# Optimization experiments

Hardware: AMD Instinct MI355X
Metric: run time of the kernel (lower is better)

The kernel has to match this reference:

```python
import jax, jax.numpy as jnp
import numpy as np

DIM = 1024
HEADS = 32
HEAD_DIM = DIM // HEADS
SR_RATIO = 2
N_RATIO = SR_RATIO * SR_RATIO  # AvgPool1d kernel/stride
BN_EPS = 1e-6


def setup_inputs() -> dict:
    key = jax.random.key(0)
    ks = jax.random.split(key, 10)
    B, N, C = 4, 2048, DIM
    s = C ** -0.5
    return {
        "x": jax.random.normal(ks[0], (B, N, C), dtype=jnp.float32),
        # torch.nn.Linear weights, shape [out, in]; applied as x @ W.T
        "Wq": jax.random.normal(ks[1], (C, C), dtype=jnp.float32) * s,
        "Wk": jax.random.normal(ks[2], (C, C), dtype=jnp.float32) * s,
        "Wv": jax.random.normal(ks[3], (C, C), dtype=jnp.float32) * s,
        "Wp": jax.random.normal(ks[4], (C, C), dtype=jnp.float32) * s,
        "bp": jax.random.normal(ks[5], (C,), dtype=jnp.float32) * 0.01,
        # BatchNorm1d (eval mode) affine + running stats over channel dim C
        "bn_gamma": jnp.ones((C,), dtype=jnp.float32),
        "bn_beta": jnp.zeros((C,), dtype=jnp.float32),
        "bn_mean": jax.random.normal(ks[6], (C,), dtype=jnp.float32) * 0.01,
        "bn_var": jnp.ones((C,), dtype=jnp.float32) + jax.random.uniform(ks[7], (C,), dtype=jnp.float32) * 0.1,
    }


def reference(x, Wq, Wk, Wv, Wp, bp, bn_gamma, bn_beta, bn_mean, bn_var):
    B, N, C = x.shape
    scale = HEAD_DIM ** -0.5
    # Q from full-resolution tokens
    q = (x @ Wq.T).reshape(B, N, HEADS, HEAD_DIM).transpose(0, 2, 1, 3)  # [B,H,N,d]
    # spatial reduction: AvgPool1d(kernel=N_RATIO, stride=N_RATIO) over tokens
    xr = x.reshape(B, N // N_RATIO, N_RATIO, C).mean(axis=2)  # [B,M,C]
    # BatchNorm1d eval: normalize channel dim with running stats
    xr = (xr - bn_mean) * jax.lax.rsqrt(bn_var + BN_EPS) * bn_gamma + bn_beta
    M = xr.shape[1]
    k = (xr @ Wk.T).reshape(B, M, HEADS, HEAD_DIM).transpose(0, 2, 1, 3)  # [B,H,M,d]
    v = (xr @ Wv.T).reshape(B, M, HEADS, HEAD_DIM).transpose(0, 2, 1, 3)  # [B,H,M,d]
    # NOTE: no softmax in the original module — raw scaled scores feed the second matmul
    attn = jnp.einsum("bhnd,bhmd->bhnm", q, k) * scale  # [B,H,N,M]
    out = jnp.einsum("bhnm,bhmd->bhnd", attn, v)        # [B,H,N,d]
    out = out.transpose(0, 2, 1, 3).reshape(B, N, C)
    return out @ Wp.T + bp
```

## Files before the change

### kernel.cpp

```cpp
#include <hip/hip_runtime.h>
#include <stdint.h>

#define DEVFN __device__ __forceinline__

typedef __attribute__((ext_vector_type(8))) short s16x8;
typedef __attribute__((ext_vector_type(4))) float f32x4;

DEVFN float bf2f(uint16_t u) {
  union { uint32_t i; float f; } v; v.i = ((uint32_t)u) << 16; return v.f;
}
DEVFN uint16_t f2bf(float f) {
  union { float f; uint32_t i; } v; v.f = f;
  uint32_t u = v.i;
  return (uint16_t)((u + 0x7FFFu + ((u >> 16) & 1u)) >> 16);
}

DEVFN void gload_lds16(const void* g, void* l) {
  __builtin_amdgcn_global_load_lds(
      (const __attribute__((address_space(1))) uint32_t*)g,
      (__attribute__((address_space(3))) uint32_t*)l, 16, 0, 0);
}

__global__ __launch_bounds__(256)
void prep_kernel(const float* __restrict__ x,
                 const float* __restrict__ bn_g, const float* __restrict__ bn_b,
                 const float* __restrict__ bn_m, const float* __restrict__ bn_v,
                 const float* __restrict__ Wk, const float* __restrict__ Wv,
                 const float* __restrict__ Wp,
                 uint16_t* __restrict__ Xh,
                 uint16_t* __restrict__ XRh,
                 uint16_t* __restrict__ Wkvh,
                 uint16_t* __restrict__ Wph)
{
  const int t = threadIdx.x;
  const int bid = blockIdx.x;
  if (bid < 2048) {
    const int prow = bid;
    const int c0 = t * 4;
    const size_t xbase = (size_t)prow * 4096 + c0;
    float s[4] = {0.f, 0.f, 0.f, 0.f};
#pragma unroll
    for (int r = 0; r < 4; ++r) {
      const float4 w = *(const float4*)(x + xbase + (size_t)r * 1024);
      const float vv[4] = { w.x, w.y, w.z, w.w };
      uint64_t wh = 0;
#pragma unroll
      for (int j = 0; j < 4; ++j) {
        wh |= ((uint64_t)f2bf(vv[j])) << (16 * j);
        s[j] += vv[j];
      }
      *(uint64_t*)(Xh + xbase + (size_t)r * 1024) = wh;
    }
    uint64_t wh = 0;
#pragma unroll
    for (int j = 0; j < 4; ++j) {
      const int c = c0 + j;
      const float y = (s[j] * 0.25f - bn_m[c]) / sqrtf(bn_v[c] + 1e-6f) * bn_g[c] + bn_b[c];
      wh |= ((uint64_t)f2bf(y)) << (16 * j);
    }
    *(uint64_t*)(XRh + (size_t)prow * 1024 + c0) = wh;
  } else {
    const int wb = bid - 2048;
    const int which = wb >> 10;
    const int i = (wb & 1023) * 256 + t;
    const float* src = (which == 0) ? Wk : (which == 1) ? Wv : Wp;
    const float4 v = ((const float4*)src)[i];
    const float vv[4] = { v.x, v.y, v.z, v.w };
    uint64_t wh = 0;
#pragma unroll
    for (int j = 0; j < 4; ++j)
      wh |= ((uint64_t)f2bf(vv[j])) << (16 * j);
    if (which == 2) {
      ((uint64_t*)Wph)[i] = wh;
    } else {
      ((uint64_t*)Wkvh)[(size_t)which * (1024 * 1024 / 4) + i] = wh;
    }
  }
}

template<bool BATCHB, bool AMODA, int EPI, bool KSPLIT2>
__global__ __launch_bounds__(256, 3)
void gemm_nt(const uint16_t* __restrict__ A0,
             const uint16_t* __restrict__ B0,
             float* __restrict__ C32, uint16_t* __restrict__ Cb0,
             const float* __restrict__ bias,
             int M, int N, int K, int rows_per_batch)
{
  constexpr int BM = 64, BN = 128, BK = 128;
  constexpr int NREP = 2;
  constexpr int APASS = 4;
  constexpr int BPASS = 8;
  __shared__ uint16_t sA[BM * BK];
  __shared__ uint16_t sB[BN * BK];

  const int t = threadIdx.x;
  const int lane = t & 63;
  const int wc = t >> 6;
  const int fq = lane >> 4, fr = lane & 15;

  const int nwg = gridDim.x;
  const int cpx = nwg >> 3;
  const int orig = blockIdx.x;
  const int swz = (orig & 7) * cpx + (orig >> 3);
  const int nbx = N >> 7;
  const int bm = (swz / nbx) * BM;
  const int bn = (swz % nbx) * BN;

  const uint16_t* Ap = A0;
  const uint16_t* Bp = B0;
  if (BATCHB)
    Bp += (size_t)(bm / rows_per_batch) * (size_t)N * (size_t)K;
  if (KSPLIT2) {
    const size_t half = (size_t)blockIdx.y * M * N;
    if (EPI == 1) Cb0 += half; else C32 += half;
  }

  f32x4 acc[4][NREP];
#pragma unroll
  for (int m = 0; m < 4; ++m)
#pragma unroll
    for (int n = 0; n < NREP; ++n) acc[m][n] = (f32x4)0.0f;

  const int nkt = K >> (KSPLIT2 ? 8 : 7);
  const int kt0 = KSPLIT2 ? (blockIdx.y * nkt) : 0;
  for (int kt = kt0; kt < kt0 + nkt; ++kt) {
    __syncthreads();
#pragma unroll
    for (int i = 0; i < APASS; ++i) {
      const int X = t * 16 + i * 4096;
      const int r = X >> 8;
      const int g = ((X >> 4) & 15) ^ (r & 7);
      const int kcol = (kt << 7) + g * 8;
      const int arow = AMODA ? ((bm + r) & 1023) : (bm + r);
      gload_lds16(Ap + (size_t)arow * K + kcol, (char*)(&sA[0]) + X);
    }
#pragma unroll
    for (int i = 0; i < BPASS; ++i) {
      const int X = t * 16 + i * 4096;
      const int r = X >> 8;
      const int g = ((X >> 4) & 15) ^ (r & 7);
      const int kcol = (kt << 7) + g * 8;
      gload_lds16(Bp + (size_t)(bn + r) * K + kcol, (char*)(&sB[0]) + X);
    }
    __syncthreads();
#pragma unroll
    for (int ks = 0; ks < 4; ++ks) {
      s16x8 av[4], bv[NREP];
#pragma unroll
      for (int m = 0; m < 4; ++m) {
        const int ra = m * 16 + fr;
        const int offA = ra * 256 + ((((ks << 2) + fq) ^ (ra & 7)) << 4);
        av[m] = *(const s16x8*)((const char*)(&sA[0]) + offA);
      }
#pragma unroll
      for (int n = 0; n < NREP; ++n) {
        const int rb = wc * 32 + n * 16 + fr;
        const int offB = rb * 256 + ((((ks << 2) + fq) ^ (rb & 7)) << 4);
        bv[n] = *(const s16x8*)((const char*)(&sB[0]) + offB);
      }
#pragma unroll
      for (int m = 0; m < 4; ++m)
#pragma unroll
        for (int n = 0; n < NREP; ++n)
          acc[m][n] = __builtin_amdgcn_mfma_f32_16x16x32_bf16(
              av[m], bv[n], acc[m][n], 0, 0, 0);
    }
  }

#pragma unroll
  for (int m = 0; m < 4; ++m) {
#pragma unroll
    for (int n = 0; n < NREP; ++n) {
#pragma unroll
      for (int j = 0; j < 4; ++j) {
        const int row = bm + m * 16 + fq * 4 + j;
        const int col = bn + wc * 32 + n * 16 + fr;
        const size_t idx = (size_t)row * N + col;
        float v = acc[m][n][j];
        if constexpr (EPI == 0) {
          C32[idx] = v;
        } else if constexpr (EPI == 1) {
          Cb0[idx] = f2bf(v);
        } else {
          C32[idx] = v + bias[col];
        }
      }
    }
  }
}

__global__ __launch_bounds__(256)
void kv1_kernel(const uint16_t* __restrict__ KVcat, float* __restrict__ part)
{
  const int bid = blockIdx.x;
  const int bh = bid >> 3, ch = bid & 7;
  const int b = bh >> 5, h = bh & 31;
  const int t = threadIdx.x;
  __shared__ float sK[64][32];
  __shared__ float sV[64][32];
  const int f = t >> 3, e0 = (t & 7) * 4;
  const int lr = t >> 2, q = t & 3;
  const size_t rowb = (size_t)(b * 512 + ch * 64 + lr) * 2048 + h * 32 + q * 8;
  const size_t H = (size_t)2048 * 2048;
  const s16x8 k0 = *(const s16x8*)(KVcat + rowb);
  const s16x8 k1 = *(const s16x8*)(KVcat + H + rowb);
  const s16x8 v0 = *(const s16x8*)(KVcat + rowb + 1024);
  const s16x8 v1 = *(const s16x8*)(KVcat + H + rowb + 1024);
#pragma unroll
  for (int j = 0; j < 8; ++j) {
    sK[lr][q * 8 + j] = bf2f((uint16_t)k0[j]) + bf2f((uint16_t)k1[j]);
    sV[lr][q * 8 + j] = bf2f((uint16_t)v0[j]) + bf2f((uint16_t)v1[j]);
  }
  __syncthreads();
  float a0 = 0.f, a1 = 0.f, a2 = 0.f, a3 = 0.f;
#pragma unroll 16
  for (int mm = 0; mm < 64; ++mm) {
    const float kf = sK[mm][f];
    const float4 vv = *(const float4*)&sV[mm][e0];
    a0 += kf * vv.x; a1 += kf * vv.y; a2 += kf * vv.z; a3 += kf * vv.w;
  }
  float* o = part + ((size_t)bid * 32 + f) * 32 + e0;
  o[0] = a0; o[1] = a1; o[2] = a2; o[3] = a3;
}

__global__ __launch_bounds__(256)
void t_kernel(const float* __restrict__ part, const float* __restrict__ Wq,
              uint16_t* __restrict__ Tth)
{
  const int bid = blockIdx.x;
  const int b = bid >> 7, h = (bid >> 2) & 31, cc = bid & 3;
  const int bh = b * 32 + h;
  const int t = threadIdx.x;
  __shared__ float sKV[32][32];
  {
    const int f = t >> 3, e0 = (t & 7) * 4;
    f32x4 a = (f32x4)0.0f;
#pragma unroll
    for (int ch = 0; ch < 8; ++ch)
      a += *(const f32x4*)(part + ((size_t)(bh * 8 + ch) * 32 + f) * 32 + e0);
    a *= 0.17677669529663687f;
    *(f32x4*)&sKV[f][e0] = a;
  }
  __syncthreads();
  const int c = cc * 256 + t;
  f32x4 acc[8];
#pragma unroll
  for (int i = 0; i < 8; ++i) acc[i] = (f32x4)0.0f;
  const float* wqp = Wq + (size_t)(h * 32) * 1024 + c;
#pragma unroll 8
  for (int f = 0; f < 32; ++f) {
    const float wq = wqp[(size_t)f * 1024];
#pragma unroll
    for (int i = 0; i < 8; ++i) {
      const f32x4 kv = *(const f32x4*)&sKV[f][i * 4];
      acc[i] += kv * wq;
    }
  }
  const size_t o = (((size_t)b << 10) + c) * 1024 + h * 32;
#pragma unroll
  for (int i = 0; i < 8; ++i) {
    uint64_t wh = 0;
#pragma unroll
    for (int j = 0; j < 4; ++j)
      wh |= ((uint64_t)f2bf(acc[i][j])) << (16 * j);
    *(uint64_t*)(Tth + o + i * 4) = wh;
  }
}

extern "C" void kernel_launch(void* const* d_in, const int* in_sizes, int n_in,
                              void* d_out, int out_size, void* d_ws, size_t ws_size,
                              hipStream_t stream)
{
  const float* x   = (const float*)d_in[0];
  const float* Wq  = (const float*)d_in[1];
  const float* Wk  = (const float*)d_in[2];
  const float* Wv  = (const float*)d_in[3];
  const float* Wp  = (const float*)d_in[4];
  const float* bp  = (const float*)d_in[5];
  const float* bng = (const float*)d_in[6];
  const float* bnb = (const float*)d_in[7];
  const float* bnm = (const float*)d_in[8];
  const float* bnv = (const float*)d_in[9];
  float* out = (float*)d_out;

  char* ws = (char*)d_ws;
  size_t off = 0;
  auto alloc = [&](size_t bytes) {
    char* p = ws + off;
    off += (bytes + 255) & ~(size_t)255;
    return p;
  };
  uint16_t* Xh   = (uint16_t*)alloc((size_t)8192 * 1024 * 2);
  uint16_t* XRh  = (uint16_t*)alloc((size_t)2048 * 1024 * 2);
  uint16_t* Wkvh = (uint16_t*)alloc((size_t)2048 * 1024 * 2);
  uint16_t* Wph  = (uint16_t*)alloc((size_t)1024 * 1024 * 2);
  uint16_t* KVcat= (uint16_t*)alloc((size_t)2 * 2048 * 2048 * 2);
  uint16_t* Gh   = (uint16_t*)alloc((size_t)4096 * 1024 * 2);
  uint16_t* Tth = KVcat;
  float* KVpart = (float*)Gh;

  prep_kernel<<<5120, 256, 0, stream>>>(x, bng, bnb, bnm, bnv, Wk, Wv, Wp,
                                        Xh, XRh, Wkvh, Wph);
  gemm_nt<false, false, 1, true><<<dim3(512, 2), 256, 0, stream>>>(
      XRh, Wkvh, nullptr, KVcat, nullptr,
      2048, 2048, 1024, 1 << 30);
  kv1_kernel<<<1024, 256, 0, stream>>>(KVcat, KVpart);
  t_kernel<<<512, 256, 0, stream>>>(KVpart, Wq, Tth);
  gemm_nt<true, true, 1, false><<<512, 256, 0, stream>>>(
      Wph, Tth, nullptr, Gh, nullptr,
      4096, 1024, 1024, 1024);
  gemm_nt<true, false, 2, false><<<1024, 256, 0, stream>>>(
      Xh, Gh, out, nullptr, bp,
      8192, 1024, 1024, 2048);
}
```

Baseline: 94.26 us.

## Use 128-row GEMM tiles and overlap next-tile loads with MFMA compute

The GEMM kernel gains a SMALLM template option. The large GEMMs now use 128x128 tiles split across a 2x2 wave grid, while the small GEMM keeps 64-row tiles. The main loop now reads all fragments for a k-tile from LDS into registers, then issues the global-to-LDS loads for the next k-tile before running the MFMAs, so memory traffic overlaps with compute. The cost is more registers per thread (launch bounds lowered from 3 to 2 blocks per CU) and half as many workgroups on the 128-row launches.

```diff
diff --git a/kernel.cpp b/kernel.cpp
--- a/kernel.cpp
+++ b/kernel.cpp
@@ -78,24 +78,27 @@
   }
 }
 
-template<bool BATCHB, bool AMODA, int EPI, bool KSPLIT2>
-__global__ __launch_bounds__(256, 3)
+template<bool BATCHB, bool AMODA, int EPI, bool KSPLIT2, bool SMALLM>
+__global__ __launch_bounds__(256, 2)
 void gemm_nt(const uint16_t* __restrict__ A0,
              const uint16_t* __restrict__ B0,
              float* __restrict__ C32, uint16_t* __restrict__ Cb0,
              const float* __restrict__ bias,
              int M, int N, int K, int rows_per_batch)
 {
-  constexpr int BM = 64, BN = 128, BK = 128;
-  constexpr int NREP = 2;
-  constexpr int APASS = 4;
+  constexpr int BM = SMALLM ? 64 : 128, BN = 128, BK = 128;
+  constexpr int WCN = SMALLM ? 4 : 2;
+  constexpr int WNW = BN / WCN;
+  constexpr int NREP = WNW / 16;
+  constexpr int APASS = SMALLM ? 4 : 8;
   constexpr int BPASS = 8;
   __shared__ uint16_t sA[BM * BK];
   __shared__ uint16_t sB[BN * BK];
 
   const int t = threadIdx.x;
   const int lane = t & 63;
-  const int wc = t >> 6;
+  const int wave = t >> 6;
+  const int wr = wave / WCN, wc = wave % WCN;
   const int fq = lane >> 4, fr = lane & 15;
 
   const int nwg = gridDim.x;
@@ -121,10 +124,7 @@
 #pragma unroll
     for (int n = 0; n < NREP; ++n) acc[m][n] = (f32x4)0.0f;
 
-  const int nkt = K >> (KSPLIT2 ? 8 : 7);
-  const int kt0 = KSPLIT2 ? (blockIdx.y * nkt) : 0;
-  for (int kt = kt0; kt < kt0 + nkt; ++kt) {
-    __syncthreads();
+  auto STAGE = [&](int kt) {
 #pragma unroll
     for (int i = 0; i < APASS; ++i) {
       const int X = t * 16 + i * 4096;
@@ -142,29 +142,44 @@
       const int kcol = (kt << 7) + g * 8;
       gload_lds16(Bp + (size_t)(bn + r) * K + kcol, (char*)(&sB[0]) + X);
     }
+  };
+
+  const int nkt = K >> (KSPLIT2 ? 8 : 7);
+  const int kt0 = KSPLIT2 ? (blockIdx.y * nkt) : 0;
+  const int ktend = kt0 + nkt;
+
+  STAGE(kt0);
+  for (int kt = kt0; kt < ktend; ++kt) {
     __syncthreads();
+
+    s16x8 av[4][4], bv[4][NREP];
 #pragma unroll
     for (int ks = 0; ks < 4; ++ks) {
-      s16x8 av[4], bv[NREP];
 #pragma unroll
       for (int m = 0; m < 4; ++m) {
-        const int ra = m * 16 + fr;
+        const int ra = wr * 64 + m * 16 + fr;
         const int offA = ra * 256 + ((((ks << 2) + fq) ^ (ra & 7)) << 4);
-        av[m] = *(const s16x8*)((const char*)(&sA[0]) + offA);
+        av[ks][m] = *(const s16x8*)((const char*)(&sA[0]) + offA);
       }
 #pragma unroll
       for (int n = 0; n < NREP; ++n) {
-        const int rb = wc * 32 + n * 16 + fr;
+        const int rb = wc * WNW + n * 16 + fr;
         const int offB = rb * 256 + ((((ks << 2) + fq) ^ (rb & 7)) << 4);
-        bv[n] = *(const s16x8*)((const char*)(&sB[0]) + offB);
+        bv[ks][n] = *(const s16x8*)((const char*)(&sB[0]) + offB);
       }
+    }
+
+    __syncthreads();
+    if (kt + 1 < ktend) STAGE(kt + 1);
+
+#pragma unroll
+    for (int ks = 0; ks < 4; ++ks)
 #pragma unroll
       for (int m = 0; m < 4; ++m)
 #pragma unroll
         for (int n = 0; n < NREP; ++n)
           acc[m][n] = __builtin_amdgcn_mfma_f32_16x16x32_bf16(
-              av[m], bv[n], acc[m][n], 0, 0, 0);
-    }
+              av[ks][m], bv[ks][n], acc[m][n], 0, 0, 0);
   }
 
 #pragma unroll
@@ -173,8 +188,8 @@
     for (int n = 0; n < NREP; ++n) {
 #pragma unroll
       for (int j = 0; j < 4; ++j) {
-        const int row = bm + m * 16 + fq * 4 + j;
-        const int col = bn + wc * 32 + n * 16 + fr;
+        const int row = bm + wr * 64 + m * 16 + fq * 4 + j;
+        const int col = bn + wc * WNW + n * 16 + fr;
         const size_t idx = (size_t)row * N + col;
         float v = acc[m][n][j];
         if constexpr (EPI == 0) {
@@ -301,15 +316,15 @@
 
   prep_kernel<<<5120, 256, 0, stream>>>(x, bng, bnb, bnm, bnv, Wk, Wv, Wp,
                                         Xh, XRh, Wkvh, Wph);
-  gemm_nt<false, false, 1, true><<<dim3(512, 2), 256, 0, stream>>>(
+  gemm_nt<false, false, 1, true, false><<<dim3(256, 2), 256, 0, stream>>>(
       XRh, Wkvh, nullptr, KVcat, nullptr,
       2048, 2048, 1024, 1 << 30);
   kv1_kernel<<<1024, 256, 0, stream>>>(KVcat, KVpart);
   t_kernel<<<512, 256, 0, stream>>>(KVpart, Wq, Tth);
-  gemm_nt<true, true, 1, false><<<512, 256, 0, stream>>>(
+  gemm_nt<true, true, 1, false, true><<<512, 256, 0, stream>>>(
       Wph, Tth, nullptr, Gh, nullptr,
       4096, 1024, 1024, 1024);
-  gemm_nt<true, false, 2, false><<<1024, 256, 0, stream>>>(
+  gemm_nt<true, false, 2, false, false><<<512, 256, 0, stream>>>(
       Xh, Gh, out, nullptr, bp,
       8192, 1024, 1024, 2048);
 }
```

Result: faster. 85.47 us (-9.3%).
